# Kernel optimization log

Hardware: AMD Instinct MI355X
Metric: run time of the kernel (lower is better)

## Reference

```python
import jax, jax.numpy as jnp
import numpy as np


def setup_inputs() -> dict:
    key = jax.random.key(0)
    k1, k2, k3, k4, k5 = jax.random.split(key, 5)
    B, D, U = 16384, 512, 512
    scale = 1.0 / np.sqrt(D + U)
    return {
        "inputs": jax.random.normal(k1, (B, D), dtype=jnp.float32),
        "h_prev": jax.random.normal(k2, (B, U), dtype=jnp.float32),
        "Wz": jax.random.normal(k3, (D + U, U), dtype=jnp.float32) * scale,
        "Wr": jax.random.normal(k4, (D + U, U), dtype=jnp.float32) * scale,
        "Wh": jax.random.normal(k5, (D + U, U), dtype=jnp.float32) * scale,
    }


def reference(inputs, h_prev, Wz, Wr, Wh):
    # x_h: [B, D+U]
    x_h = jnp.concatenate([inputs, h_prev], axis=-1)
    z = jax.nn.sigmoid(x_h @ Wz)                     # update gate [B, U]
    r = jax.nn.sigmoid(x_h @ Wr)                     # reset gate  [B, U]
    h_hat = jnp.tanh(jnp.concatenate([inputs, r * h_prev], axis=-1) @ Wh)
    new_h = z * h_prev + (1.0 - z) * h_hat
    return new_h
```

## Files before the change

### kernel.cpp

```cpp
#include <hip/hip_runtime.h>
#include <hip/hip_bf16.h>
#include <stdint.h>

typedef __attribute__((ext_vector_type(8))) short short8;
typedef __attribute__((ext_vector_type(4))) float f32x4;
typedef unsigned short u16;

#define AS1 __attribute__((address_space(1)))
#define AS3 __attribute__((address_space(3)))

__device__ __forceinline__ u16 f2b(float f) {
  union { float f; uint32_t u; } c; c.f = f;
  uint32_t u = c.u;
  return (u16)((u + 0x7fffu + ((u >> 16) & 1u)) >> 16);
}
__device__ __forceinline__ float b2f(u16 b) {
  union { uint32_t u; float f; } c; c.u = ((uint32_t)b) << 16;
  return c.f;
}


__global__ void cvt_bf16_kernel(const float* __restrict__ src,
                                u16* __restrict__ dst, int n4) {
  int i = blockIdx.x * blockDim.x + threadIdx.x;
  if (i >= n4) return;
  const float4 v = reinterpret_cast<const float4*>(src)[i];
  ushort4 o;
  o.x = f2b(v.x); o.y = f2b(v.y); o.z = f2b(v.z); o.w = f2b(v.w);
  reinterpret_cast<ushort4*>(dst)[i] = o;
}

__global__ void cvt_transpose_kernel(const float* __restrict__ w0,
                                     const float* __restrict__ w1,
                                     const float* __restrict__ w2,
                                     u16* __restrict__ d0,
                                     u16* __restrict__ d1,
                                     u16* __restrict__ d2,
                                     int K, int N) {
  const float* src = (blockIdx.y == 0) ? w0 : (blockIdx.y == 1 ? w1 : w2);
  u16* dst = (blockIdx.y == 0) ? d0 : (blockIdx.y == 1 ? d1 : d2);
  int idx = blockIdx.x * blockDim.x + threadIdx.x;
  if (idx >= K * N) return;
  int k = idx / N, n = idx - k * N;
  dst[(size_t)n * K + k] = f2b(src[idx]);
}

__device__ __forceinline__ void stage_tile(const u16* __restrict__ src, int stride,
                                           u16* lds, int wid, int lane) {
#pragma unroll
  for (int j = 0; j < 2; ++j) {
    const int lds_e = wid * 1024 + j * 512;
    const int e = lds_e + lane * 8;
    const int row = e >> 5;
    const int kk = e & 31;
    __builtin_amdgcn_global_load_lds(
        (const AS1 void*)(src + (size_t)row * stride + kk),
        (AS3 void*)(lds + lds_e), 16, 0, 0);
  }
}

__global__ __launch_bounds__(256, 2) void gru_gates_kernel(
    const u16* __restrict__ xb,
    const u16* __restrict__ hb,
    const u16* __restrict__ wzt,
    const u16* __restrict__ wrt,
    const float* __restrict__ hprev,
    u16* __restrict__ zb, u16* __restrict__ rhb) {
  __shared__ u16 As[128 * 32];
  __shared__ u16 Bz[128 * 32];
  __shared__ u16 Br[128 * 32];
  const int tid = threadIdx.x, lane = tid & 63, wid = tid >> 6;
  const int wr = wid >> 1, wc = wid & 1;
  const int bm = blockIdx.y, bn = blockIdx.x;

  f32x4 accz[4][4] = {};
  f32x4 accr[4][4] = {};

  for (int k0 = 0; k0 < 1024; k0 += 32) {
    const u16* asrc = (k0 < 512) ? (xb + (size_t)bm * 128 * 512 + k0)
                                 : (hb + (size_t)bm * 128 * 512 + (k0 - 512));
    stage_tile(asrc, 512, As, wid, lane);
    stage_tile(wzt + (size_t)bn * 128 * 1024 + k0, 1024, Bz, wid, lane);
    stage_tile(wrt + (size_t)bn * 128 * 1024 + k0, 1024, Br, wid, lane);
    __syncthreads();

    short8 a[4], bz[4], br[4];
    const int koff = (lane >> 4) * 8;
    const int rsel = lane & 15;
#pragma unroll
    for (int m = 0; m < 4; ++m)
      a[m] = *reinterpret_cast<const short8*>(&As[(wr * 64 + m * 16 + rsel) * 32 + koff]);
#pragma unroll
    for (int n = 0; n < 4; ++n) {
      bz[n] = *reinterpret_cast<const short8*>(&Bz[(wc * 64 + n * 16 + rsel) * 32 + koff]);
      br[n] = *reinterpret_cast<const short8*>(&Br[(wc * 64 + n * 16 + rsel) * 32 + koff]);
    }
#pragma unroll
    for (int m = 0; m < 4; ++m)
#pragma unroll
      for (int n = 0; n < 4; ++n) {
        accz[m][n] = __builtin_amdgcn_mfma_f32_16x16x32_bf16(a[m], bz[n], accz[m][n], 0, 0, 0);
        accr[m][n] = __builtin_amdgcn_mfma_f32_16x16x32_bf16(a[m], br[n], accr[m][n], 0, 0, 0);
      }
    __syncthreads();
  }

  const int col0 = bn * 128 + wc * 64 + (lane & 15);
  const int row0 = bm * 128 + wr * 64 + (lane >> 4) * 4;
#pragma unroll
  for (int m = 0; m < 4; ++m)
#pragma unroll
    for (int n = 0; n < 4; ++n)
#pragma unroll
      for (int q = 0; q < 4; ++q) {
        const int row = row0 + m * 16 + q;
        const int col = col0 + n * 16;
        const size_t idx = (size_t)row * 512 + col;
        const float z = 1.f / (1.f + __expf(-accz[m][n][q]));
        const float r = 1.f / (1.f + __expf(-accr[m][n][q]));
        const float h = hprev[idx];
        zb[idx] = f2b(z);
        rhb[idx] = f2b(r * h);
      }
}

__global__ __launch_bounds__(256, 2) void gru_cand_kernel(
    const u16* __restrict__ xb,
    const u16* __restrict__ rhb,
    const u16* __restrict__ wht,
    const float* __restrict__ hprev,
    const u16* __restrict__ zb,
    float* __restrict__ out) {
  __shared__ u16 As[128 * 32];
  __shared__ u16 Bs[128 * 32];
  const int tid = threadIdx.x, lane = tid & 63, wid = tid >> 6;
  const int wr = wid >> 1, wc = wid & 1;
  const int bm = blockIdx.y, bn = blockIdx.x;

  f32x4 acc[4][4] = {};

  for (int k0 = 0; k0 < 1024; k0 += 32) {
    const u16* asrc = (k0 < 512) ? (xb + (size_t)bm * 128 * 512 + k0)
                                 : (rhb + (size_t)bm * 128 * 512 + (k0 - 512));
    stage_tile(asrc, 512, As, wid, lane);
    stage_tile(wht + (size_t)bn * 128 * 1024 + k0, 1024, Bs, wid, lane);
    __syncthreads();

    short8 a[4], b[4];
    const int koff = (lane >> 4) * 8;
    const int rsel = lane & 15;
#pragma unroll
    for (int m = 0; m < 4; ++m)
      a[m] = *reinterpret_cast<const short8*>(&As[(wr * 64 + m * 16 + rsel) * 32 + koff]);
#pragma unroll
    for (int n = 0; n < 4; ++n)
      b[n] = *reinterpret_cast<const short8*>(&Bs[(wc * 64 + n * 16 + rsel) * 32 + koff]);
#pragma unroll
    for (int m = 0; m < 4; ++m)
#pragma unroll
      for (int n = 0; n < 4; ++n)
        acc[m][n] = __builtin_amdgcn_mfma_f32_16x16x32_bf16(a[m], b[n], acc[m][n], 0, 0, 0);
    __syncthreads();
  }

  const int col0 = bn * 128 + wc * 64 + (lane & 15);
  const int row0 = bm * 128 + wr * 64 + (lane >> 4) * 4;
#pragma unroll
  for (int m = 0; m < 4; ++m)
#pragma unroll
    for (int n = 0; n < 4; ++n)
#pragma unroll
      for (int q = 0; q < 4; ++q) {
        const int row = row0 + m * 16 + q;
        const int col = col0 + n * 16;
        const size_t idx = (size_t)row * 512 + col;
        const float s = acc[m][n][q];
        const float hh = 2.f / (1.f + __expf(-2.f * s)) - 1.f;
        const float z = b2f(zb[idx]);
        const float h = hprev[idx];
        out[idx] = z * h + (1.f - z) * hh;
      }
}

extern "C" void kernel_launch(void* const* d_in, const int* in_sizes, int n_in,
                              void* d_out, int out_size, void* d_ws, size_t ws_size,
                              hipStream_t stream) {
  const float* inputs = (const float*)d_in[0];
  const float* h_prev = (const float*)d_in[1];
  const float* Wz = (const float*)d_in[2];
  const float* Wr = (const float*)d_in[3];
  const float* Wh = (const float*)d_in[4];
  float* out = (float*)d_out;

  const int B = 16384, D = 512, U = 512, K = 1024;

  u16* xb = (u16*)d_ws;
  u16* hb = xb + (size_t)B * D;
  u16* wzt = hb + (size_t)B * U;
  u16* wrt = wzt + (size_t)K * U;
  u16* wht = wrt + (size_t)K * U;
  u16* zb = wht + (size_t)K * U;
  u16* rhb = zb + (size_t)B * U;

  const int n4 = (B * D) / 4;
  cvt_bf16_kernel<<<(n4 + 255) / 256, 256, 0, stream>>>(inputs, xb, n4);
  cvt_bf16_kernel<<<(n4 + 255) / 256, 256, 0, stream>>>(h_prev, hb, n4);
  dim3 tg((K * U + 255) / 256, 3);
  cvt_transpose_kernel<<<tg, 256, 0, stream>>>(Wz, Wr, Wh, wzt, wrt, wht, K, U);

  dim3 g(U / 128, B / 128);
  gru_gates_kernel<<<g, 256, 0, stream>>>(xb, hb, wzt, wrt, h_prev, zb, rhb);
  gru_cand_kernel<<<g, 256, 0, stream>>>(xb, rhb, wht, h_prev, zb, out);
}
```

Baseline: 116.0 us.

## Replace GRU GEMMs with triple-buffered swizzled 256-row tile kernel

Replaces the two single-buffered 128x128 GEMM kernels with one templated kernel using 512 threads, 256-row tiles, a three-stage global_load_lds pipeline with explicit vmcnt waits, XOR-swizzled LDS layout, an XCD-aware block remap and raised wave priority around the MFMAs. The gates pass treats Wz and Wr as one contiguous 1024-column weight matrix (wzt then wrt in the workspace), so each block computes either z or r columns. The changes aim to hide load latency, remove LDS bank conflicts and improve operand reuse. In exchange the kernel relies on the workspace layout, on hand-tuned wait counts, and runs with fewer, larger blocks (256 per launch).

```diff
diff --git a/kernel.cpp b/kernel.cpp
--- a/kernel.cpp
+++ b/kernel.cpp
@@ -18,7 +18,6 @@
   union { uint32_t u; float f; } c; c.u = ((uint32_t)b) << 16;
   return c.f;
 }
-
 
 __global__ void cvt_bf16_kernel(const float* __restrict__ src,
                                 u16* __restrict__ dst, int n4) {
@@ -45,141 +44,148 @@
   dst[(size_t)n * K + k] = f2b(src[idx]);
 }
 
-__device__ __forceinline__ void stage_tile(const u16* __restrict__ src, int stride,
-                                           u16* lds, int wid, int lane) {
-#pragma unroll
-  for (int j = 0; j < 2; ++j) {
-    const int lds_e = wid * 1024 + j * 512;
-    const int e = lds_e + lane * 8;
-    const int row = e >> 5;
-    const int kk = e & 31;
-    __builtin_amdgcn_global_load_lds(
-        (const AS1 void*)(src + (size_t)row * stride + kk),
-        (AS3 void*)(lds + lds_e), 16, 0, 0);
+
+#define BAR() do { __builtin_amdgcn_s_barrier(); __builtin_amdgcn_sched_barrier(0); } while (0)
+#define VMW(n) asm volatile("s_waitcnt vmcnt(" #n ")" ::: "memory")
+
+template <int BN, int EPI>
+__global__ __launch_bounds__(512, 1) void gemm_kernel(
+    const u16* __restrict__ a1,
+    const u16* __restrict__ a2,
+    const u16* __restrict__ wt,
+    const float* __restrict__ hprev,
+    const u16* __restrict__ zb_in,
+    u16* __restrict__ o_z,
+    u16* __restrict__ o_rh,
+    float* __restrict__ o_f) {
+  constexpr int NT = 32;
+  constexpr int NF = BN / 64;
+  constexpr int ATILE_E = 8192;
+  constexpr int BTILE_E = BN * 32;
+  constexpr int BUF_E = ATILE_E + BTILE_E;
+
+  __shared__ u16 lds[3 * BUF_E];
+
+  const int tid = threadIdx.x;
+  const int lane = tid & 63;
+  const int wid = tid >> 6;
+  const int wm = wid >> 2;
+  const int wn = wid & 3;
+
+  const int wg = ((int)blockIdx.x & 7) * 32 + ((int)blockIdx.x >> 3);
+  const int bn = wg & 3;
+  const int bm = wg >> 2;
+
+  const int srow = wid * 16 + (lane >> 2);
+  const int scol = ((lane & 3) ^ ((lane >> 3) & 3)) << 4;
+  const size_t aoff = (size_t)srow * 1024 + scol;
+  const size_t boff = (size_t)srow * 2048 + scol;
+  const size_t abase_g = (size_t)bm * 262144;
+  const size_t bbase_g = (size_t)bn * BN * 2048;
+
+  auto STAGE = [&](int ktn, u16* buf) {
+    const char* asn = (ktn < 16) ? ((const char*)a1 + abase_g + (size_t)ktn * 64)
+                                 : ((const char*)a2 + abase_g + (size_t)(ktn - 16) * 64);
+    const char* bsn = (const char*)wt + bbase_g + (size_t)ktn * 64;
+    __builtin_amdgcn_global_load_lds((const AS1 void*)(asn + aoff),
+                                     (AS3 void*)(buf + wid * 512), 16, 0, 0);
+    __builtin_amdgcn_global_load_lds((const AS1 void*)(asn + 131072 + aoff),
+                                     (AS3 void*)(buf + 4096 + wid * 512), 16, 0, 0);
+    __builtin_amdgcn_global_load_lds((const AS1 void*)(bsn + boff),
+                                     (AS3 void*)(buf + ATILE_E + wid * 512), 16, 0, 0);
+    if constexpr (BN == 256)
+      __builtin_amdgcn_global_load_lds((const AS1 void*)(bsn + 262144 + boff),
+                                       (AS3 void*)(buf + ATILE_E + 4096 + wid * 512), 16, 0, 0);
+  };
+
+  const int rsel = lane & 15;
+  const int kg = lane >> 4;
+  const int rcol = (kg ^ ((rsel >> 1) & 3)) << 4;
+  const int abyte = (wm * 128 + rsel) * 64 + rcol;
+  const int bbyte = 16384 + (wn * (BN / 4) + rsel) * 64 + rcol;
+
+  f32x4 acc[8][NF] = {};
+
+  STAGE(0, lds);
+  STAGE(1, lds + BUF_E);
+  if constexpr (BN == 256) VMW(4); else VMW(3);
+  BAR();
+
+  int cb = 0;
+  for (int kt = 0; kt < NT; ++kt) {
+    u16* cur = lds + cb * BUF_E;
+    const bool st = (kt + 2) < NT;
+    if (st) {
+      int nb = cb + 2; if (nb >= 3) nb -= 3;
+      STAGE(kt + 2, lds + nb * BUF_E);
+    }
+    short8 bv[NF];
+#pragma unroll
+    for (int nf = 0; nf < NF; ++nf)
+      bv[nf] = *(const short8*)((const char*)cur + bbyte + nf * 1024);
+    __builtin_amdgcn_s_setprio(1);
+#pragma unroll
+    for (int mf = 0; mf < 8; ++mf) {
+      const short8 av = *(const short8*)((const char*)cur + abyte + mf * 1024);
+#pragma unroll
+      for (int nf = 0; nf < NF; ++nf)
+        acc[mf][nf] = __builtin_amdgcn_mfma_f32_16x16x32_bf16(av, bv[nf], acc[mf][nf], 0, 0, 0);
+    }
+    __builtin_amdgcn_s_setprio(0);
+    if (st) {
+      if constexpr (BN == 256) VMW(4); else VMW(3);
+    } else {
+      VMW(0);
+    }
+    BAR();
+    ++cb; if (cb == 3) cb = 0;
   }
-}
-
-__global__ __launch_bounds__(256, 2) void gru_gates_kernel(
-    const u16* __restrict__ xb,
-    const u16* __restrict__ hb,
-    const u16* __restrict__ wzt,
-    const u16* __restrict__ wrt,
-    const float* __restrict__ hprev,
-    u16* __restrict__ zb, u16* __restrict__ rhb) {
-  __shared__ u16 As[128 * 32];
-  __shared__ u16 Bz[128 * 32];
-  __shared__ u16 Br[128 * 32];
-  const int tid = threadIdx.x, lane = tid & 63, wid = tid >> 6;
-  const int wr = wid >> 1, wc = wid & 1;
-  const int bm = blockIdx.y, bn = blockIdx.x;
-
-  f32x4 accz[4][4] = {};
-  f32x4 accr[4][4] = {};
-
-  for (int k0 = 0; k0 < 1024; k0 += 32) {
-    const u16* asrc = (k0 < 512) ? (xb + (size_t)bm * 128 * 512 + k0)
-                                 : (hb + (size_t)bm * 128 * 512 + (k0 - 512));
-    stage_tile(asrc, 512, As, wid, lane);
-    stage_tile(wzt + (size_t)bn * 128 * 1024 + k0, 1024, Bz, wid, lane);
-    stage_tile(wrt + (size_t)bn * 128 * 1024 + k0, 1024, Br, wid, lane);
-    __syncthreads();
-
-    short8 a[4], bz[4], br[4];
-    const int koff = (lane >> 4) * 8;
-    const int rsel = lane & 15;
-#pragma unroll
-    for (int m = 0; m < 4; ++m)
-      a[m] = *reinterpret_cast<const short8*>(&As[(wr * 64 + m * 16 + rsel) * 32 + koff]);
-#pragma unroll
-    for (int n = 0; n < 4; ++n) {
-      bz[n] = *reinterpret_cast<const short8*>(&Bz[(wc * 64 + n * 16 + rsel) * 32 + koff]);
-      br[n] = *reinterpret_cast<const short8*>(&Br[(wc * 64 + n * 16 + rsel) * 32 + koff]);
-    }
-#pragma unroll
-    for (int m = 0; m < 4; ++m)
-#pragma unroll
-      for (int n = 0; n < 4; ++n) {
-        accz[m][n] = __builtin_amdgcn_mfma_f32_16x16x32_bf16(a[m], bz[n], accz[m][n], 0, 0, 0);
-        accr[m][n] = __builtin_amdgcn_mfma_f32_16x16x32_bf16(a[m], br[n], accr[m][n], 0, 0, 0);
-      }
-    __syncthreads();
+
+  const int row0 = bm * 256 + wm * 128 + kg * 4;
+  const int col0 = bn * BN + wn * (BN / 4) + rsel;
+  if constexpr (EPI == 0) {
+    if (bn < 2) {
+#pragma unroll
+      for (int mf = 0; mf < 8; ++mf)
+#pragma unroll
+        for (int nf = 0; nf < NF; ++nf)
+#pragma unroll
+          for (int q = 0; q < 4; ++q) {
+            const int row = row0 + mf * 16 + q;
+            const int col = col0 + nf * 16;
+            const float zf = 1.f / (1.f + __expf(-acc[mf][nf][q]));
+            o_z[(size_t)row * 512 + col] = f2b(zf);
+          }
+    } else {
+#pragma unroll
+      for (int mf = 0; mf < 8; ++mf)
+#pragma unroll
+        for (int nf = 0; nf < NF; ++nf)
+#pragma unroll
+          for (int q = 0; q < 4; ++q) {
+            const int row = row0 + mf * 16 + q;
+            const int col = col0 + nf * 16 - 512;
+            const size_t idx = (size_t)row * 512 + col;
+            const float rf = 1.f / (1.f + __expf(-acc[mf][nf][q]));
+            o_rh[idx] = f2b(rf * hprev[idx]);
+          }
+    }
+  } else {
+#pragma unroll
+    for (int mf = 0; mf < 8; ++mf)
+#pragma unroll
+      for (int nf = 0; nf < NF; ++nf)
+#pragma unroll
+        for (int q = 0; q < 4; ++q) {
+          const int row = row0 + mf * 16 + q;
+          const int col = col0 + nf * 16;
+          const size_t idx = (size_t)row * 512 + col;
+          const float s = acc[mf][nf][q];
+          const float hh = 2.f / (1.f + __expf(-2.f * s)) - 1.f;
+          const float z = b2f(zb_in[idx]);
+          o_f[idx] = z * hprev[idx] + (1.f - z) * hh;
+        }
   }
-
-  const int col0 = bn * 128 + wc * 64 + (lane & 15);
-  const int row0 = bm * 128 + wr * 64 + (lane >> 4) * 4;
-#pragma unroll
-  for (int m = 0; m < 4; ++m)
-#pragma unroll
-    for (int n = 0; n < 4; ++n)
-#pragma unroll
-      for (int q = 0; q < 4; ++q) {
-        const int row = row0 + m * 16 + q;
-        const int col = col0 + n * 16;
-        const size_t idx = (size_t)row * 512 + col;
-        const float z = 1.f / (1.f + __expf(-accz[m][n][q]));
-        const float r = 1.f / (1.f + __expf(-accr[m][n][q]));
-        const float h = hprev[idx];
-        zb[idx] = f2b(z);
-        rhb[idx] = f2b(r * h);
-      }
-}
-
-__global__ __launch_bounds__(256, 2) void gru_cand_kernel(
-    const u16* __restrict__ xb,
-    const u16* __restrict__ rhb,
-    const u16* __restrict__ wht,
-    const float* __restrict__ hprev,
-    const u16* __restrict__ zb,
-    float* __restrict__ out) {
-  __shared__ u16 As[128 * 32];
-  __shared__ u16 Bs[128 * 32];
-  const int tid = threadIdx.x, lane = tid & 63, wid = tid >> 6;
-  const int wr = wid >> 1, wc = wid & 1;
-  const int bm = blockIdx.y, bn = blockIdx.x;
-
-  f32x4 acc[4][4] = {};
-
-  for (int k0 = 0; k0 < 1024; k0 += 32) {
-    const u16* asrc = (k0 < 512) ? (xb + (size_t)bm * 128 * 512 + k0)
-                                 : (rhb + (size_t)bm * 128 * 512 + (k0 - 512));
-    stage_tile(asrc, 512, As, wid, lane);
-    stage_tile(wht + (size_t)bn * 128 * 1024 + k0, 1024, Bs, wid, lane);
-    __syncthreads();
-
-    short8 a[4], b[4];
-    const int koff = (lane >> 4) * 8;
-    const int rsel = lane & 15;
-#pragma unroll
-    for (int m = 0; m < 4; ++m)
-      a[m] = *reinterpret_cast<const short8*>(&As[(wr * 64 + m * 16 + rsel) * 32 + koff]);
-#pragma unroll
-    for (int n = 0; n < 4; ++n)
-      b[n] = *reinterpret_cast<const short8*>(&Bs[(wc * 64 + n * 16 + rsel) * 32 + koff]);
-#pragma unroll
-    for (int m = 0; m < 4; ++m)
-#pragma unroll
-      for (int n = 0; n < 4; ++n)
-        acc[m][n] = __builtin_amdgcn_mfma_f32_16x16x32_bf16(a[m], b[n], acc[m][n], 0, 0, 0);
-    __syncthreads();
-  }
-
-  const int col0 = bn * 128 + wc * 64 + (lane & 15);
-  const int row0 = bm * 128 + wr * 64 + (lane >> 4) * 4;
-#pragma unroll
-  for (int m = 0; m < 4; ++m)
-#pragma unroll
-    for (int n = 0; n < 4; ++n)
-#pragma unroll
-      for (int q = 0; q < 4; ++q) {
-        const int row = row0 + m * 16 + q;
-        const int col = col0 + n * 16;
-        const size_t idx = (size_t)row * 512 + col;
-        const float s = acc[m][n][q];
-        const float hh = 2.f / (1.f + __expf(-2.f * s)) - 1.f;
-        const float z = b2f(zb[idx]);
-        const float h = hprev[idx];
-        out[idx] = z * h + (1.f - z) * hh;
-      }
 }
 
 extern "C" void kernel_launch(void* const* d_in, const int* in_sizes, int n_in,
@@ -208,7 +214,6 @@
   dim3 tg((K * U + 255) / 256, 3);
   cvt_transpose_kernel<<<tg, 256, 0, stream>>>(Wz, Wr, Wh, wzt, wrt, wht, K, U);
 
-  dim3 g(U / 128, B / 128);
-  gru_gates_kernel<<<g, 256, 0, stream>>>(xb, hb, wzt, wrt, h_prev, zb, rhb);
-  gru_cand_kernel<<<g, 256, 0, stream>>>(xb, rhb, wht, h_prev, zb, out);
-}
+  gemm_kernel<256, 0><<<dim3(256), 512, 0, stream>>>(xb, hb, wzt, h_prev, nullptr, zb, rhb, nullptr);
+  gemm_kernel<128, 1><<<dim3(256), 512, 0, stream>>>(xb, rhb, wht, h_prev, zb, nullptr, nullptr, out);
+}
```

After: 106.7 us. -8.0%, faster.
